# Kernel tuning notes

Measured on AMD Instinct MI355X. Metric: run time of the kernel, lower is better.

## Reference

```python
import jax, jax.numpy as jnp
import numpy as np

N_BRANCHES = 4
BATCH = 8192
DIM = 4096
NUM_CLASSES = 1024
MARGIN = 0.3
EPS = 1e-8


def setup_inputs() -> dict:
    key = jax.random.key(0)
    branch_feats = jax.random.normal(key, (N_BRANCHES, BATCH, DIM), dtype=jnp.float32)
    # every class appears BATCH // NUM_CLASSES = 8 times (>1, so no detach branch)
    targets = jnp.arange(BATCH, dtype=jnp.int32) % NUM_CLASSES
    return {"branch_feats": branch_feats, "targets": targets, "num_classes": NUM_CLASSES}


def _centers(branch_feats, targets, num_classes):
    # masked per-class mean == segment mean (torch.unique over 0..C-1, sorted)
    counts = jax.ops.segment_sum(jnp.ones(branch_feats.shape[1], jnp.float32),
                                 targets, num_segments=num_classes)  # [C]
    sums = jax.vmap(lambda f: jax.ops.segment_sum(f, targets, num_segments=num_classes))(
        branch_feats)  # [N, C, D]
    return sums / counts[None, :, None]


def reference(branch_feats, targets, num_classes):
    centers = _centers(branch_feats, targets, num_classes)  # [N, C, D]
    C = num_classes

    # hard negative per (branch, class): min_{l != k} ||c[k] - c[l]||
    sq = jnp.sum(centers * centers, axis=-1)                 # [N, C]
    gram = jnp.einsum('nkd,nld->nkl', centers, centers)      # [N, C, C]
    d2 = jnp.maximum(sq[:, :, None] + sq[:, None, :] - 2.0 * gram, 0.0)
    dist = jnp.sqrt(d2)                                      # [N, C, C]
    dist = jnp.where(jnp.eye(C, dtype=bool)[None], jnp.inf, dist)
    hard_neg = jnp.min(dist, axis=-1)                        # [N, C]

    # positive distances for each unordered branch pair i < j
    ii, jj = jnp.triu_indices(N_BRANCHES, k=1)
    # F.pairwise_distance adds eps to the difference before the norm
    pos = jnp.linalg.norm(centers[ii] - centers[jj] + EPS, axis=-1)  # [P, C]

    # loss += relu(margin + pos_dist[k] - hard_neg_i[k]); valid_pairs = P * C
    return jnp.mean(jax.nn.relu(MARGIN + pos - hard_neg[ii]))
```

## Files before the change

### kernel.cpp

```cpp
#include <hip/hip_runtime.h>

#define N_BR   4
#define BATCH  8192
#define DIM    4096
#define NCLS   1024
#define MARGIN 0.3f
#define EPS_P  1e-8f
#define MAXPC  16

typedef __attribute__((ext_vector_type(4))) float f32x4;
typedef __attribute__((ext_vector_type(8))) short short8;
typedef unsigned short u16;
typedef unsigned char u8;

struct alignas(8) U16x4 { u16 x, y, z, w; };

__device__ __forceinline__ u16 f2bf(float x) {
  unsigned u = __float_as_uint(x);
  u += 0x7FFFu + ((u >> 16) & 1u);
  return (u16)(u >> 16);
}
__device__ __forceinline__ float bf2f(u16 h) {
  return __uint_as_float(((unsigned)h) << 16);
}

__global__ __launch_bounds__(256) void prepk(
    const int* __restrict__ targets, int* __restrict__ members,
    int* __restrict__ cnt, unsigned int* __restrict__ hn) {
  __shared__ int cnt_s[4], off_s[5];
  int c = blockIdx.x, tid = threadIdx.x;
  int w = tid >> 6, lane = tid & 63;
  if (tid < N_BR) hn[tid * NCLS + c] = 0x7F800000u;
  int cn = 0;
  for (int i = 0; i < (BATCH / 4) / 64; ++i) {
    int b = w * (BATCH / 4) + i * 64 + lane;
    cn += __popcll(__ballot(targets[b] == c));
  }
  if (lane == 0) cnt_s[w] = cn;
  __syncthreads();
  if (tid == 0) {
    off_s[0] = 0;
    for (int i = 0; i < 4; ++i) off_s[i + 1] = off_s[i] + cnt_s[i];
    cnt[c] = off_s[4];
  }
  __syncthreads();
  int pos = off_s[w];
  for (int i = 0; i < (BATCH / 4) / 64; ++i) {
    int b = w * (BATCH / 4) + i * 64 + lane;
    bool hit = (targets[b] == c);
    unsigned long long m = __ballot(hit);
    if (hit) {
      int p = pos + __popcll(m & ((1ULL << lane) - 1ULL));
      if (p < MAXPC) members[c * MAXPC + p] = b;
    }
    pos += __popcll(m);
  }
}

__global__ __launch_bounds__(256) void centersk(
    const float* __restrict__ feats, const int* __restrict__ members,
    const int* __restrict__ cnt, u16* __restrict__ cbf,
    u8* __restrict__ cq, float* __restrict__ sq) {
  int c = blockIdx.x, n = blockIdx.y, tid = threadIdx.x;
  int count = cnt[c]; if (count > MAXPC) count = MAXPC;
  int beg = c * MAXPC, end = beg + count;
  float inv = 1.0f / (float)count;
  const float* fb = feats + (size_t)n * BATCH * DIM;
  size_t cbase = ((size_t)n * NCLS + c) * DIM;
  float ssq = 0.f;
#pragma unroll
  for (int it = 0; it < DIM / 1024; ++it) {
    int d = (it * 256 + tid) * 4;
    f32x4 acc = {0.f, 0.f, 0.f, 0.f};
    for (int m = beg; m < end; ++m) {
      int b = members[m];
      f32x4 v = *(const f32x4*)(fb + (size_t)b * DIM + d);
      acc += v;
    }
    f32x4 ctr = acc * inv;
    U16x4 h;
    h.x = f2bf(ctr.x); h.y = f2bf(ctr.y); h.z = f2bf(ctr.z); h.w = f2bf(ctr.w);
    *(U16x4*)(cbf + cbase + d) = h;
    int packed = 0;
    packed = __builtin_amdgcn_cvt_pk_fp8_f32(ctr.x, ctr.y, packed, false);
    packed = __builtin_amdgcn_cvt_pk_fp8_f32(ctr.z, ctr.w, packed, true);
    *(int*)(cq + cbase + d) = packed;
    ssq += ctr.x * ctr.x + ctr.y * ctr.y + ctr.z * ctr.z + ctr.w * ctr.w;
  }
  for (int off = 1; off < 64; off <<= 1) ssq += __shfl_xor(ssq, off, 64);
  __shared__ float rs[4];
  if ((tid & 63) == 0) rs[tid >> 6] = ssq;
  __syncthreads();
  if (tid == 0) sq[n * NCLS + c] = rs[0] + rs[1] + rs[2] + rs[3];
}

__global__ __launch_bounds__(256) void gramk(
    const u8* __restrict__ cq, const float* __restrict__ sq,
    unsigned int* __restrict__ hn) {
  __shared__ u8 As[2][64 * 64];
  __shared__ u8 Bs[2][64 * 64];
  int x = (blockIdx.x & 7) * 17 + (blockIdx.x >> 3);
  int n = blockIdx.y;
  int ti = 0;
  while (x >= 16 - ti) { x -= 16 - ti; ++ti; }
  int tj = ti + x;
  int tid = threadIdx.x;
  int wid = tid >> 6, lane = tid & 63;
  int wr = wid >> 1, wc = wid & 1;
  int r0 = ti * 64, c0 = tj * 64;
  const u8* base = cq + (size_t)n * NCLS * DIM;

  f32x4 acc[2][2] = {};

#define STAGE(buf, kb)                                                          \
  {                                                                             \
    int g = tid;                              \
    int row_ = g >> 2, c16_ = g & 3;                                            \
    int sc16_ = c16_ ^ ((row_ >> 1) & 3);        \
    const u8* gA_ = base + (size_t)(r0 + row_) * DIM + (kb) + sc16_ * 16;       \
    const u8* gB_ = base + (size_t)(c0 + row_) * DIM + (kb) + sc16_ * 16;       \
    __builtin_amdgcn_global_load_lds(                                           \
        (const __attribute__((address_space(1))) void*)gA_,                     \
        (__attribute__((address_space(3))) void*)(As[buf] + g * 16), 16, 0, 0); \
    __builtin_amdgcn_global_load_lds(                                           \
        (const __attribute__((address_space(1))) void*)gB_,                     \
        (__attribute__((address_space(3))) void*)(Bs[buf] + g * 16), 16, 0, 0); \
  }

#define COMPUTE(buf)                                                            \
  {                                                                             \
    _Pragma("unroll")                                                           \
    for (int ks = 0; ks < 2; ++ks) {                                            \
      long a_[2], b_[2];                                                        \
      int co_ = ks * 4 + (lane >> 4);         \
      _Pragma("unroll")                                                         \
      for (int mi = 0; mi < 2; ++mi) {                                          \
        int r_ = wr * 32 + mi * 16 + (lane & 15);                               \
        int p_ = ((r_ >> 1) & 3) << 1;                                          \
        a_[mi] = *(const long*)(As[buf] + r_ * 64 + (co_ ^ p_) * 8);            \
      }                                                                         \
      _Pragma("unroll")                                                         \
      for (int nj = 0; nj < 2; ++nj) {                                          \
        int r_ = wc * 32 + nj * 16 + (lane & 15);                               \
        int p_ = ((r_ >> 1) & 3) << 1;                                          \
        b_[nj] = *(const long*)(Bs[buf] + r_ * 64 + (co_ ^ p_) * 8);            \
      }                                                                         \
      _Pragma("unroll")                                                         \
      for (int mi = 0; mi < 2; ++mi)                                            \
        _Pragma("unroll")                                                       \
        for (int nj = 0; nj < 2; ++nj)                                          \
          acc[mi][nj] = __builtin_amdgcn_mfma_f32_16x16x32_fp8_fp8(             \
              a_[mi], b_[nj], acc[mi][nj], 0, 0, 0);                            \
    }                                                                           \
  }

  STAGE(0, 0);
  __syncthreads();
  int cur = 0;
  for (int kb = 64; kb < DIM; kb += 64) {
    STAGE(cur ^ 1, kb);
    COMPUTE(cur);
    __syncthreads();
    cur ^= 1;
  }
  COMPUTE(cur);
#undef STAGE
#undef COMPUTE

  const float* sqn = sq + n * NCLS;
  unsigned int* hb = hn + n * NCLS;
  int grp = lane >> 4, lid = lane & 15;
  float d2v[2][2][4];
#pragma unroll
  for (int mi = 0; mi < 2; ++mi)
#pragma unroll
    for (int nj = 0; nj < 2; ++nj)
#pragma unroll
      for (int j = 0; j < 4; ++j) {
        int rr = r0 + wr * 32 + mi * 16 + grp * 4 + j;
        int cc = c0 + wc * 32 + nj * 16 + lid;
        float d2 = fmaxf(sqn[rr] + sqn[cc] - 2.0f * acc[mi][nj][j], 0.f);
        d2v[mi][nj][j] = (rr == cc) ? __builtin_inff() : d2;
      }
#pragma unroll
  for (int mi = 0; mi < 2; ++mi)
#pragma unroll
    for (int j = 0; j < 4; ++j) {
      float dmin = fminf(d2v[mi][0][j], d2v[mi][1][j]);
#pragma unroll
      for (int off = 1; off < 16; off <<= 1)
        dmin = fminf(dmin, __shfl_xor(dmin, off, 64));
      if (lid == 0) {
        int rr = r0 + wr * 32 + mi * 16 + grp * 4 + j;
        atomicMin(&hb[rr], __float_as_uint(dmin));
      }
    }
#pragma unroll
  for (int nj = 0; nj < 2; ++nj) {
    float cmin = __builtin_inff();
#pragma unroll
    for (int mi = 0; mi < 2; ++mi)
#pragma unroll
      for (int j = 0; j < 4; ++j)
        cmin = fminf(cmin, d2v[mi][nj][j]);
    cmin = fminf(cmin, __shfl_xor(cmin, 16, 64));
    cmin = fminf(cmin, __shfl_xor(cmin, 32, 64));
    if (grp == 0) {
      int cc = c0 + wc * 32 + nj * 16 + lid;
      atomicMin(&hb[cc], __float_as_uint(cmin));
    }
  }
}

__global__ __launch_bounds__(256) void posk(
    const u16* __restrict__ cbf, const unsigned int* __restrict__ hn,
    float* __restrict__ partial) {
  int c = blockIdx.x, tid = threadIdx.x;
  const int ii[6] = {0, 0, 0, 1, 1, 2};
  const int jj[6] = {1, 2, 3, 2, 3, 3};
  float s[6] = {0.f, 0.f, 0.f, 0.f, 0.f, 0.f};
#pragma unroll
  for (int it = 0; it < DIM / 2048; ++it) {
    int d = (it * 256 + tid) * 8;
    float v[N_BR][8];
#pragma unroll
    for (int nb = 0; nb < N_BR; ++nb) {
      short8 h = *(const short8*)(cbf + ((size_t)nb * NCLS + c) * DIM + d);
#pragma unroll
      for (int e = 0; e < 8; ++e) v[nb][e] = bf2f((u16)h[e]);
    }
#pragma unroll
    for (int p = 0; p < 6; ++p) {
#pragma unroll
      for (int e = 0; e < 8; ++e) {
        float df = v[ii[p]][e] - v[jj[p]][e] + EPS_P;
        s[p] += df * df;
      }
    }
  }
  __shared__ float red[4][6];
#pragma unroll
  for (int p = 0; p < 6; ++p) {
    float x = s[p];
    for (int off = 1; off < 64; off <<= 1) x += __shfl_xor(x, off, 64);
    if ((tid & 63) == 0) red[tid >> 6][p] = x;
  }
  __syncthreads();
  if (tid == 0) {
    float total = 0.f;
#pragma unroll
    for (int p = 0; p < 6; ++p) {
      float sum = red[0][p] + red[1][p] + red[2][p] + red[3][p];
      float pos = sqrtf(sum);
      float hneg = sqrtf(__uint_as_float(hn[ii[p] * NCLS + c]));
      float t = MARGIN + pos - hneg;
      total += fmaxf(t, 0.f);
    }
    partial[c] = total;
  }
}

__global__ void finalk(const float* __restrict__ partial, float* __restrict__ out) {
  int tid = threadIdx.x;
  float s = 0.f;
  for (int c = tid; c < NCLS; c += 256) s += partial[c];
  for (int off = 1; off < 64; off <<= 1) s += __shfl_xor(s, off, 64);
  __shared__ float rs[4];
  if ((tid & 63) == 0) rs[tid >> 6] = s;
  __syncthreads();
  if (tid == 0) out[0] = (rs[0] + rs[1] + rs[2] + rs[3]) * (1.0f / (6.0f * NCLS));
}

extern "C" void kernel_launch(void* const* d_in, const int* in_sizes, int n_in,
                              void* d_out, int out_size, void* d_ws, size_t ws_size,
                              hipStream_t stream) {
  const float* feats = (const float*)d_in[0];
  const int* targets = (const int*)d_in[1];
  float* out = (float*)d_out;
  char* ws = (char*)d_ws;

  int* members     = (int*)(ws + 0);
  int* cnt         = (int*)(ws + 65536);
  float* sq        = (float*)(ws + 69632);
  unsigned int* hn = (unsigned int*)(ws + 86016);
  float* partial   = (float*)(ws + 102400);
  u16* cbf         = (u16*)(ws + 131072);
  u8* cq           = (u8*)(ws + 131072 + 33554432);

  hipLaunchKernelGGL(prepk, dim3(NCLS), dim3(256), 0, stream,
                     targets, members, cnt, hn);
  hipLaunchKernelGGL(centersk, dim3(NCLS, N_BR), dim3(256), 0, stream,
                     feats, members, cnt, cbf, cq, sq);
  hipLaunchKernelGGL(gramk, dim3(136, N_BR), dim3(256), 0, stream, cq, sq, hn);
  hipLaunchKernelGGL(posk, dim3(NCLS), dim3(256), 0, stream, cbf, hn, partial);
  hipLaunchKernelGGL(finalk, dim3(1), dim3(256), 0, stream, partial, out);
}
```

Before: 174.7 us.

## Fuse class-member scan into centers, drop bf16 copy, deepen gram pipeline

The separate prep kernel is folded into the centers kernel: each block scans targets itself and keeps the member list in shared memory, which removes one launch and the global members/cnt buffers at the cost of every branch repeating the scan. The bf16 center copy is removed and the positive-distance kernel now reads the fp8 centers, which cuts write and read traffic but lowers precision of the positive distances. The gram kernel moves from a double-buffered loop to a 4-stage LDS ring with explicit vmcnt waits, so more global loads are in flight.

```diff
diff --git a/kernel.cpp b/kernel.cpp
--- a/kernel.cpp
+++ b/kernel.cpp
@@ -9,28 +9,22 @@
 #define MAXPC  16
 
 typedef __attribute__((ext_vector_type(4))) float f32x4;
-typedef __attribute__((ext_vector_type(8))) short short8;
+typedef __attribute__((ext_vector_type(2))) float f32x2;
+typedef __attribute__((ext_vector_type(4))) int i32x4;
 typedef unsigned short u16;
 typedef unsigned char u8;
 
-struct alignas(8) U16x4 { u16 x, y, z, w; };
-
-__device__ __forceinline__ u16 f2bf(float x) {
-  unsigned u = __float_as_uint(x);
-  u += 0x7FFFu + ((u >> 16) & 1u);
-  return (u16)(u >> 16);
-}
-__device__ __forceinline__ float bf2f(u16 h) {
-  return __uint_as_float(((unsigned)h) << 16);
-}
-
-__global__ __launch_bounds__(256) void prepk(
-    const int* __restrict__ targets, int* __restrict__ members,
-    int* __restrict__ cnt, unsigned int* __restrict__ hn) {
+__global__ __launch_bounds__(256) void centersk(
+    const float* __restrict__ feats, const int* __restrict__ targets,
+    u8* __restrict__ cq, float* __restrict__ sq,
+    unsigned int* __restrict__ hn) {
+  __shared__ int mem_s[MAXPC];
   __shared__ int cnt_s[4], off_s[5];
-  int c = blockIdx.x, tid = threadIdx.x;
+  __shared__ float rs[4];
+  int c = blockIdx.x, n = blockIdx.y, tid = threadIdx.x;
   int w = tid >> 6, lane = tid & 63;
-  if (tid < N_BR) hn[tid * NCLS + c] = 0x7F800000u;
+  if (tid == 0) hn[n * NCLS + c] = 0x7F800000u;
+
   int cn = 0;
   for (int i = 0; i < (BATCH / 4) / 64; ++i) {
     int b = w * (BATCH / 4) + i * 64 + lane;
@@ -41,7 +35,6 @@
   if (tid == 0) {
     off_s[0] = 0;
     for (int i = 0; i < 4; ++i) off_s[i + 1] = off_s[i] + cnt_s[i];
-    cnt[c] = off_s[4];
   }
   __syncthreads();
   int pos = off_s[w];
@@ -51,20 +44,14 @@
     unsigned long long m = __ballot(hit);
     if (hit) {
       int p = pos + __popcll(m & ((1ULL << lane) - 1ULL));
-      if (p < MAXPC) members[c * MAXPC + p] = b;
+      if (p < MAXPC) mem_s[p] = b;
     }
     pos += __popcll(m);
   }
-}
-
-__global__ __launch_bounds__(256) void centersk(
-    const float* __restrict__ feats, const int* __restrict__ members,
-    const int* __restrict__ cnt, u16* __restrict__ cbf,
-    u8* __restrict__ cq, float* __restrict__ sq) {
-  int c = blockIdx.x, n = blockIdx.y, tid = threadIdx.x;
-  int count = cnt[c]; if (count > MAXPC) count = MAXPC;
-  int beg = c * MAXPC, end = beg + count;
+  __syncthreads();
+  int count = off_s[4]; if (count > MAXPC) count = MAXPC;
   float inv = 1.0f / (float)count;
+
   const float* fb = feats + (size_t)n * BATCH * DIM;
   size_t cbase = ((size_t)n * NCLS + c) * DIM;
   float ssq = 0.f;
@@ -72,15 +59,12 @@
   for (int it = 0; it < DIM / 1024; ++it) {
     int d = (it * 256 + tid) * 4;
     f32x4 acc = {0.f, 0.f, 0.f, 0.f};
-    for (int m = beg; m < end; ++m) {
-      int b = members[m];
+    for (int m = 0; m < count; ++m) {
+      int b = mem_s[m];
       f32x4 v = *(const f32x4*)(fb + (size_t)b * DIM + d);
       acc += v;
     }
     f32x4 ctr = acc * inv;
-    U16x4 h;
-    h.x = f2bf(ctr.x); h.y = f2bf(ctr.y); h.z = f2bf(ctr.z); h.w = f2bf(ctr.w);
-    *(U16x4*)(cbf + cbase + d) = h;
     int packed = 0;
     packed = __builtin_amdgcn_cvt_pk_fp8_f32(ctr.x, ctr.y, packed, false);
     packed = __builtin_amdgcn_cvt_pk_fp8_f32(ctr.z, ctr.w, packed, true);
@@ -88,7 +72,6 @@
     ssq += ctr.x * ctr.x + ctr.y * ctr.y + ctr.z * ctr.z + ctr.w * ctr.w;
   }
   for (int off = 1; off < 64; off <<= 1) ssq += __shfl_xor(ssq, off, 64);
-  __shared__ float rs[4];
   if ((tid & 63) == 0) rs[tid >> 6] = ssq;
   __syncthreads();
   if (tid == 0) sq[n * NCLS + c] = rs[0] + rs[1] + rs[2] + rs[3];
@@ -97,8 +80,8 @@
 __global__ __launch_bounds__(256) void gramk(
     const u8* __restrict__ cq, const float* __restrict__ sq,
     unsigned int* __restrict__ hn) {
-  __shared__ u8 As[2][64 * 64];
-  __shared__ u8 Bs[2][64 * 64];
+  __shared__ u8 As[4][64 * 64];
+  __shared__ u8 Bs[4][64 * 64];
   int x = (blockIdx.x & 7) * 17 + (blockIdx.x >> 3);
   int n = blockIdx.y;
   int ti = 0;
@@ -116,7 +99,7 @@
   {                                                                             \
     int g = tid;                              \
     int row_ = g >> 2, c16_ = g & 3;                                            \
-    int sc16_ = c16_ ^ ((row_ >> 1) & 3);        \
+    int sc16_ = c16_ ^ ((row_ >> 1) & 3);    \
     const u8* gA_ = base + (size_t)(r0 + row_) * DIM + (kb) + sc16_ * 16;       \
     const u8* gB_ = base + (size_t)(c0 + row_) * DIM + (kb) + sc16_ * 16;       \
     __builtin_amdgcn_global_load_lds(                                           \
@@ -154,16 +137,18 @@
     }                                                                           \
   }
 
+  const int NK = DIM / 64;
   STAGE(0, 0);
-  __syncthreads();
-  int cur = 0;
-  for (int kb = 64; kb < DIM; kb += 64) {
-    STAGE(cur ^ 1, kb);
-    COMPUTE(cur);
-    __syncthreads();
-    cur ^= 1;
-  }
-  COMPUTE(cur);
+  STAGE(1, 64);
+  STAGE(2, 128);
+  for (int k = 0; k < NK; ++k) {
+    if (k < NK - 2)       asm volatile("s_waitcnt vmcnt(4)" ::: "memory");
+    else if (k == NK - 2) asm volatile("s_waitcnt vmcnt(2)" ::: "memory");
+    else                  asm volatile("s_waitcnt vmcnt(0)" ::: "memory");
+    __builtin_amdgcn_s_barrier();
+    if (k + 3 < NK) STAGE((k + 3) & 3, (k + 3) * 64);
+    COMPUTE(k & 3);
+  }
 #undef STAGE
 #undef COMPUTE
 
@@ -213,30 +198,33 @@
 }
 
 __global__ __launch_bounds__(256) void posk(
-    const u16* __restrict__ cbf, const unsigned int* __restrict__ hn,
+    const u8* __restrict__ cq, const unsigned int* __restrict__ hn,
     float* __restrict__ partial) {
   int c = blockIdx.x, tid = threadIdx.x;
   const int ii[6] = {0, 0, 0, 1, 1, 2};
   const int jj[6] = {1, 2, 3, 2, 3, 3};
-  float s[6] = {0.f, 0.f, 0.f, 0.f, 0.f, 0.f};
-#pragma unroll
-  for (int it = 0; it < DIM / 2048; ++it) {
-    int d = (it * 256 + tid) * 8;
-    float v[N_BR][8];
-#pragma unroll
-    for (int nb = 0; nb < N_BR; ++nb) {
-      short8 h = *(const short8*)(cbf + ((size_t)nb * NCLS + c) * DIM + d);
-#pragma unroll
-      for (int e = 0; e < 8; ++e) v[nb][e] = bf2f((u16)h[e]);
-    }
-#pragma unroll
-    for (int p = 0; p < 6; ++p) {
-#pragma unroll
-      for (int e = 0; e < 8; ++e) {
-        float df = v[ii[p]][e] - v[jj[p]][e] + EPS_P;
-        s[p] += df * df;
-      }
-    }
+  float v[N_BR][16];
+#pragma unroll
+  for (int nb = 0; nb < N_BR; ++nb) {
+    i32x4 wds = *(const i32x4*)(cq + ((size_t)nb * NCLS + c) * DIM + tid * 16);
+#pragma unroll
+    for (int q = 0; q < 4; ++q) {
+      f32x2 lo = __builtin_amdgcn_cvt_pk_f32_fp8(wds[q], false);
+      f32x2 hi = __builtin_amdgcn_cvt_pk_f32_fp8(wds[q], true);
+      v[nb][q * 4 + 0] = lo.x; v[nb][q * 4 + 1] = lo.y;
+      v[nb][q * 4 + 2] = hi.x; v[nb][q * 4 + 3] = hi.y;
+    }
+  }
+  float s[6];
+#pragma unroll
+  for (int p = 0; p < 6; ++p) {
+    float t = 0.f;
+#pragma unroll
+    for (int e = 0; e < 16; ++e) {
+      float df = v[ii[p]][e] - v[jj[p]][e] + EPS_P;
+      t += df * df;
+    }
+    s[p] = t;
   }
   __shared__ float red[4][6];
 #pragma unroll
@@ -279,19 +267,14 @@
   float* out = (float*)d_out;
   char* ws = (char*)d_ws;
 
-  int* members     = (int*)(ws + 0);
-  int* cnt         = (int*)(ws + 65536);
-  float* sq        = (float*)(ws + 69632);
-  unsigned int* hn = (unsigned int*)(ws + 86016);
-  float* partial   = (float*)(ws + 102400);
-  u16* cbf         = (u16*)(ws + 131072);
-  u8* cq           = (u8*)(ws + 131072 + 33554432);
-
-  hipLaunchKernelGGL(prepk, dim3(NCLS), dim3(256), 0, stream,
-                     targets, members, cnt, hn);
+  float* sq        = (float*)(ws + 0);
+  unsigned int* hn = (unsigned int*)(ws + 16384);
+  float* partial   = (float*)(ws + 32768);
+  u8* cq           = (u8*)(ws + 65536);
+
   hipLaunchKernelGGL(centersk, dim3(NCLS, N_BR), dim3(256), 0, stream,
-                     feats, members, cnt, cbf, cq, sq);
+                     feats, targets, cq, sq, hn);
   hipLaunchKernelGGL(gramk, dim3(136, N_BR), dim3(256), 0, stream, cq, sq, hn);
-  hipLaunchKernelGGL(posk, dim3(NCLS), dim3(256), 0, stream, cbf, hn, partial);
+  hipLaunchKernelGGL(posk, dim3(NCLS), dim3(256), 0, stream, cq, hn, partial);
   hipLaunchKernelGGL(finalk, dim3(1), dim3(256), 0, stream, partial, out);
 }
```

Result: faster. 170.7 us (-2.3%).
